# Kernel tuning notes

Hardware: AMD Instinct MI355X
Metric: run time of the kernel (lower is better)

## Reference

```python
import jax, jax.numpy as jnp
import numpy as np

B, IN, OUT, NC, S = 4096, 512, 512, 64, 1


def setup_inputs() -> dict:
    key = jax.random.key(0)
    k = jax.random.split(key, 5)
    x = jax.random.normal(k[0], (B, IN), dtype=jnp.float32)
    centers = jax.random.normal(k[1], (NC, IN), dtype=jnp.float32)
    log_sigma = jnp.zeros((NC,), dtype=jnp.float32)
    coeff_mean = jax.random.normal(k[2], (IN, OUT, NC), dtype=jnp.float32) * 0.05
    coeff_log_var = jnp.full((IN, OUT, NC), -5.0, dtype=jnp.float32)
    base_weight = jax.random.normal(k[3], (IN, OUT), dtype=jnp.float32) * 0.05
    eps = jax.random.normal(k[4], (S, IN, OUT, NC), dtype=jnp.float32)
    return {"x": x, "centers": centers, "log_sigma": log_sigma,
            "coeff_mean": coeff_mean, "coeff_log_var": coeff_log_var,
            "base_weight": base_weight, "eps": eps}


def reference(x, centers, log_sigma, coeff_mean, coeff_log_var, base_weight, eps):
    # RBF basis: (B, NC). Original repeats this along in_features, but the
    # einsum 'bin,ion->bo' with an i-constant basis equals rbf @ coeffs.sum(i).
    dist_sq = jnp.sum((x[:, None, :] - centers[None, :, :]) ** 2, axis=-1)  # (B, NC)
    sigma = jnp.exp(log_sigma)  # (NC,)
    rbf = jnp.exp(-dist_sq / (2.0 * sigma ** 2 + 1e-8))  # (B, NC)

    # Sampled variational coefficients, reparameterized.
    std = jnp.exp(0.5 * coeff_log_var)
    coeffs = coeff_mean + eps * std            # (S, IN, OUT, NC)
    c_sum = coeffs.sum(axis=1)                 # (S, OUT, NC): sum over in_features
    n_samples = eps.shape[0]
    rbf_out = jnp.einsum('bn,son->bo', rbf, c_sum) / n_samples  # mean over samples

    out = rbf_out + x @ base_weight

    # KL vs N(0, 1) prior (prior_scale = 1.0): log(var/prior_var) = coeff_log_var
    var = jnp.exp(coeff_log_var)
    kl = 0.5 * jnp.sum(var + coeff_mean ** 2 - 1.0 - coeff_log_var)
    return out, kl
```

## Files before the change

### kernel.cpp

```cpp
#include <hip/hip_runtime.h>
#include <hip/hip_bf16.h>

#define B_SZ  4096
#define IN_F  512
#define OUT_F 512
#define NC    64
#define PAIRS 32768
#define TOT   (IN_F * PAIRS)
#define KTOT  (IN_F + NC)

typedef __attribute__((ext_vector_type(8))) short bf16x8;
typedef __attribute__((ext_vector_type(4))) float f32x4;

static __device__ inline unsigned short f2bf(float f) {
    __hip_bfloat16 h = __float2bfloat16(f);
    return *(unsigned short*)&h;
}

__global__ __launch_bounds__(1024)
void k1_partial(const float* __restrict__ cm,
                const float* __restrict__ clv,
                const float* __restrict__ eps,
                float* __restrict__ csum,
                float* __restrict__ klpart,
                int S) {
    int pb = blockIdx.x & 7;
    int rc = blockIdx.x >> 3;
    int p4 = pb * 4096 + (threadIdx.x << 2);
    size_t base = (size_t)(rc * 8) * PAIRS + p4;
    float Sf = (float)S;

    f32x4 M[8], LV[8], ES[8];
#pragma unroll
    for (int ii = 0; ii < 8; ++ii)
        M[ii] = __builtin_nontemporal_load((const f32x4*)(cm + base + (size_t)ii * PAIRS));
#pragma unroll
    for (int ii = 0; ii < 8; ++ii)
        LV[ii] = __builtin_nontemporal_load((const f32x4*)(clv + base + (size_t)ii * PAIRS));
#pragma unroll
    for (int ii = 0; ii < 8; ++ii)
        ES[ii] = __builtin_nontemporal_load((const f32x4*)(eps + base + (size_t)ii * PAIRS));
    for (int si = 1; si < S; ++si)
#pragma unroll
        for (int ii = 0; ii < 8; ++ii) {
            f32x4 e = __builtin_nontemporal_load(
                (const f32x4*)(eps + (size_t)si * TOT + base + (size_t)ii * PAIRS));
            ES[ii] += e;
        }

    f32x4 s = {0.f, 0.f, 0.f, 0.f};
    float klp = 0.f;
#pragma unroll
    for (int ii = 0; ii < 8; ++ii) {
        float e1x = __expf(0.5f * LV[ii].x);
        float e1y = __expf(0.5f * LV[ii].y);
        float e1z = __expf(0.5f * LV[ii].z);
        float e1w = __expf(0.5f * LV[ii].w);
        s.x += Sf * M[ii].x + ES[ii].x * e1x;
        s.y += Sf * M[ii].y + ES[ii].y * e1y;
        s.z += Sf * M[ii].z + ES[ii].z * e1z;
        s.w += Sf * M[ii].w + ES[ii].w * e1w;
        klp += (e1x*e1x + M[ii].x*M[ii].x - 1.f - LV[ii].x);
        klp += (e1y*e1y + M[ii].y*M[ii].y - 1.f - LV[ii].y);
        klp += (e1z*e1z + M[ii].z*M[ii].z - 1.f - LV[ii].z);
        klp += (e1w*e1w + M[ii].w*M[ii].w - 1.f - LV[ii].w);
    }

    atomicAdd(&csum[p4 + 0], s.x);
    atomicAdd(&csum[p4 + 1], s.y);
    atomicAdd(&csum[p4 + 2], s.z);
    atomicAdd(&csum[p4 + 3], s.w);

    for (int off = 32; off; off >>= 1)
        klp += __shfl_down(klp, off, 64);
    __shared__ float wsum[16];
    if ((threadIdx.x & 63) == 0) wsum[threadIdx.x >> 6] = klp;
    __syncthreads();
    if (threadIdx.x == 0) {
        float t = 0.f;
#pragma unroll
        for (int i = 0; i < 16; ++i) t += wsum[i];
        klpart[blockIdx.x] = t;
    }
}

__global__ __launch_bounds__(512)
void k_mid(const float* __restrict__ x,
           const float* __restrict__ centers,
           const float* __restrict__ log_sigma,
           const float* __restrict__ csum,
           const float* __restrict__ klpart,
           const float* __restrict__ bw,
           unsigned short* __restrict__ rbf,
           unsigned short* __restrict__ wct,
           unsigned short* __restrict__ xbf,
           float* __restrict__ kl_out,
           float inv_S) {
    __shared__ float shbuf[16 * 8 * 64];
    int bid = blockIdx.x, t = threadIdx.x;

    if (bid < 256) {
        float (*red)[8][64] = (float (*)[8][64])shbuf;
        int n = t & 63;
        int wu = __builtin_amdgcn_readfirstlane(t >> 6);
        int b0 = bid * 16;

        float creg[64];
#pragma unroll
        for (int q = 0; q < 16; ++q) {
            float4 v = *(const float4*)(centers + (size_t)n * IN_F + wu * 64 + q * 4);
            creg[q * 4 + 0] = v.x; creg[q * 4 + 1] = v.y;
            creg[q * 4 + 2] = v.z; creg[q * 4 + 3] = v.w;
        }

        float dacc[16];
#pragma unroll
        for (int bi = 0; bi < 16; ++bi) {
            const float* xr = x + (size_t)(b0 + bi) * IN_F + wu * 64;
            float d0 = 0.f, d1 = 0.f, d2 = 0.f, d3 = 0.f;
#pragma unroll
            for (int j = 0; j < 64; j += 4) {
                float t0 = xr[j + 0] - creg[j + 0];
                float t1 = xr[j + 1] - creg[j + 1];
                float t2 = xr[j + 2] - creg[j + 2];
                float t3 = xr[j + 3] - creg[j + 3];
                d0 = fmaf(t0, t0, d0); d1 = fmaf(t1, t1, d1);
                d2 = fmaf(t2, t2, d2); d3 = fmaf(t3, t3, d3);
            }
            dacc[bi] = (d0 + d1) + (d2 + d3);
        }
#pragma unroll
        for (int bi = 0; bi < 16; ++bi)
            red[bi][wu][n] = dacc[bi];
        __syncthreads();
#pragma unroll
        for (int pass = 0; pass < 2; ++pass) {
            int idx = pass * 512 + t;
            int bi = idx >> 6, nn = idx & 63;
            float ssum = 0.f;
#pragma unroll
            for (int w = 0; w < 8; ++w) ssum += red[bi][w][nn];
            float sg  = __expf(log_sigma[nn]);
            float inv = 1.f / (2.f * sg * sg + 1e-8f);
            rbf[(size_t)(b0 + bi) * NC + nn] = f2bf(__expf(-ssum * inv));
        }
    } else if (bid < 320) {
        float* tile = shbuf;
        int bb = bid - 256;
        int bi = bb >> 3, bj = bb & 7;
        int cq = t & 15, rq = t >> 4;
#pragma unroll
        for (int rr = 0; rr < 2; ++rr) {
            int row = rq * 2 + rr;
            float4 v = *(const float4*)(bw + (size_t)(bi * 64 + row) * OUT_F + bj * 64 + cq * 4);
            *(float4*)&tile[row * 68 + cq * 4] = v;
        }
        __syncthreads();
#pragma unroll
        for (int rr = 0; rr < 2; ++rr) {
            int orow = rq * 2 + rr;
            ushort4 w;
            w.x = f2bf(tile[(cq * 4 + 0) * 68 + orow]);
            w.y = f2bf(tile[(cq * 4 + 1) * 68 + orow]);
            w.z = f2bf(tile[(cq * 4 + 2) * 68 + orow]);
            w.w = f2bf(tile[(cq * 4 + 3) * 68 + orow]);
            *(ushort4*)(wct + (size_t)(bj * 64 + orow) * KTOT + bi * 64 + cq * 4) = w;
        }
    } else if (bid < 384) {
        size_t base = (size_t)(bid - 320) * 32768;
#pragma unroll
        for (int q = 0; q < 16; ++q) {
            size_t off = base + q * 2048 + t * 4;
            float4 v = *(const float4*)(x + off);
            ushort4 w = {f2bf(v.x), f2bf(v.y), f2bf(v.z), f2bf(v.w)};
            *(ushort4*)(xbf + off) = w;
        }
    } else if (bid == 384) {
        float v = klpart[t];
        for (int off = 32; off; off >>= 1)
            v += __shfl_down(v, off, 64);
        float* wsum = shbuf;
        if ((t & 63) == 0) wsum[t >> 6] = v;
        __syncthreads();
        if (t == 0) {
            float s = 0.f;
#pragma unroll
            for (int i = 0; i < 8; ++i) s += wsum[i];
            kl_out[0] = 0.5f * s;
        }
    } else {
        int p4 = (bid - 385) * 2048 + t * 4;
        float4 a = *(const float4*)(csum + p4);
        int o = p4 >> 6, n = p4 & 63;
        ushort4 w;
        w.x = f2bf(a.x * inv_S);
        w.y = f2bf(a.y * inv_S);
        w.z = f2bf(a.z * inv_S);
        w.w = f2bf(a.w * inv_S);
        *(ushort4*)(wct + (size_t)o * KTOT + IN_F + n) = w;
    }
}

__global__ __launch_bounds__(256)
void k3_mfma(const unsigned short* __restrict__ xbf,
             const unsigned short* __restrict__ rbf,
             const unsigned short* __restrict__ wct,
             float* __restrict__ out) {
    __shared__ __align__(16) unsigned short As[64 * 72];
    __shared__ __align__(16) unsigned short Bs[64 * 72];
    int t = threadIdx.x;
    int bm = blockIdx.x >> 3, bn = blockIdx.x & 7;
    int b0 = bm * 64, o0 = bn * 64;
    int ar = t & 63, ah = t >> 6;
    int lane = t & 63, wv = t >> 6;
    int fm = lane & 15, kg = lane >> 4;

    f32x4 acc[4] = {{0,0,0,0},{0,0,0,0},{0,0,0,0},{0,0,0,0}};
    const int abase = (wv * 16 + fm) * 72 + kg * 8;
    const int soff  = ar * 72 + ah * 16;

    for (int it = 0; it < 9; ++it) {
        bf16x8 av0, av1, bv0, bv1;
        if (it < 8) {
            int k0 = it * 64;
            av0 = *(const bf16x8*)(xbf + (size_t)(b0 + ar) * IN_F + k0 + ah * 16);
            av1 = *(const bf16x8*)(xbf + (size_t)(b0 + ar) * IN_F + k0 + ah * 16 + 8);
            bv0 = *(const bf16x8*)(wct + (size_t)(o0 + ar) * KTOT + k0 + ah * 16);
            bv1 = *(const bf16x8*)(wct + (size_t)(o0 + ar) * KTOT + k0 + ah * 16 + 8);
        } else {
            av0 = *(const bf16x8*)(rbf + (size_t)(b0 + ar) * NC + ah * 16);
            av1 = *(const bf16x8*)(rbf + (size_t)(b0 + ar) * NC + ah * 16 + 8);
            bv0 = *(const bf16x8*)(wct + (size_t)(o0 + ar) * KTOT + IN_F + ah * 16);
            bv1 = *(const bf16x8*)(wct + (size_t)(o0 + ar) * KTOT + IN_F + ah * 16 + 8);
        }
        __syncthreads();
        *(bf16x8*)&As[soff]     = av0;
        *(bf16x8*)&As[soff + 8] = av1;
        *(bf16x8*)&Bs[soff]     = bv0;
        *(bf16x8*)&Bs[soff + 8] = bv1;
        __syncthreads();
        bf16x8 af0 = *(bf16x8*)&As[abase];
        bf16x8 af1 = *(bf16x8*)&As[abase + 32];
#pragma unroll
        for (int nf = 0; nf < 4; ++nf) {
            bf16x8 b0f = *(bf16x8*)&Bs[(nf * 16 + fm) * 72 + kg * 8];
            acc[nf] = __builtin_amdgcn_mfma_f32_16x16x32_bf16(af0, b0f, acc[nf], 0, 0, 0);
            bf16x8 b1f = *(bf16x8*)&Bs[(nf * 16 + fm) * 72 + 32 + kg * 8];
            acc[nf] = __builtin_amdgcn_mfma_f32_16x16x32_bf16(af1, b1f, acc[nf], 0, 0, 0);
        }
    }

#pragma unroll
    for (int nf = 0; nf < 4; ++nf)
#pragma unroll
        for (int rr = 0; rr < 4; ++rr)
            out[(size_t)(b0 + wv * 16 + kg * 4 + rr) * OUT_F + o0 + nf * 16 + fm] = acc[nf][rr];
}

extern "C" void kernel_launch(void* const* d_in, const int* in_sizes, int n_in,
                              void* d_out, int out_size, void* d_ws, size_t ws_size,
                              hipStream_t stream) {
    const float* x         = (const float*)d_in[0];
    const float* centers   = (const float*)d_in[1];
    const float* log_sigma = (const float*)d_in[2];
    const float* cm        = (const float*)d_in[3];
    const float* clv       = (const float*)d_in[4];
    const float* bw        = (const float*)d_in[5];
    const float* eps       = (const float*)d_in[6];

    float* out = (float*)d_out;
    float* kl  = out + (size_t)B_SZ * OUT_F;

    float* csum   = (float*)d_ws;
    float* klpart = csum + PAIRS;
    unsigned short* wct = (unsigned short*)(klpart + 512);
    unsigned short* rbf = wct + (size_t)OUT_F * KTOT;
    unsigned short* xbf = rbf + (size_t)B_SZ * NC;

    int S = in_sizes[6] / TOT;

    hipMemsetAsync(csum, 0, PAIRS * sizeof(float), stream);
    k1_partial<<<512, 1024, 0, stream>>>(cm, clv, eps, csum, klpart, S);
    k_mid<<<401, 512, 0, stream>>>(x, centers, log_sigma, csum, klpart, bw,
                                   rbf, wct, xbf, kl, 1.0f / (float)S);
    k3_mfma<<<(B_SZ / 64) * (OUT_F / 64), 256, 0, stream>>>(xbf, rbf, wct, out);
}
```

Before: 269.4 us.

## Replace atomic accumulation of coefficient sums with per-chunk partials reduced in mid kernel

The first kernel no longer atomically adds into a zeroed coefficient-sum buffer. Each block now covers 16 input rows in two groups of 8 and writes a plain partial sum for its chunk (32 chunks) to workspace. The middle kernel gains 64 blocks that reduce the 32 partials per pair and write bf16 weights, and the memset launch goes away. This removes atomic contention and one launch, but adds about 4 MB of partial writes and reads, uses more workspace, and halves the first kernel's block size.

New measurement: 235.3 us. 12.7% less time.

```diff
diff --git a/kernel.cpp b/kernel.cpp
--- a/kernel.cpp
+++ b/kernel.cpp
@@ -8,6 +8,7 @@
 #define PAIRS 32768
 #define TOT   (IN_F * PAIRS)
 #define KTOT  (IN_F + NC)
+#define RCH   32
 
 typedef __attribute__((ext_vector_type(8))) short bf16x8;
 typedef __attribute__((ext_vector_type(4))) float f32x4;
@@ -17,69 +18,69 @@
     return *(unsigned short*)&h;
 }
 
-__global__ __launch_bounds__(1024)
+__global__ __launch_bounds__(512)
 void k1_partial(const float* __restrict__ cm,
                 const float* __restrict__ clv,
                 const float* __restrict__ eps,
-                float* __restrict__ csum,
+                float* __restrict__ part,
                 float* __restrict__ klpart,
                 int S) {
-    int pb = blockIdx.x & 7;
-    int rc = blockIdx.x >> 3;
-    int p4 = pb * 4096 + (threadIdx.x << 2);
-    size_t base = (size_t)(rc * 8) * PAIRS + p4;
+    int pb = blockIdx.x & 15;
+    int rc = blockIdx.x >> 4;
+    int p4 = pb * 2048 + (threadIdx.x << 2);
     float Sf = (float)S;
-
-    f32x4 M[8], LV[8], ES[8];
-#pragma unroll
-    for (int ii = 0; ii < 8; ++ii)
-        M[ii] = __builtin_nontemporal_load((const f32x4*)(cm + base + (size_t)ii * PAIRS));
-#pragma unroll
-    for (int ii = 0; ii < 8; ++ii)
-        LV[ii] = __builtin_nontemporal_load((const f32x4*)(clv + base + (size_t)ii * PAIRS));
-#pragma unroll
-    for (int ii = 0; ii < 8; ++ii)
-        ES[ii] = __builtin_nontemporal_load((const f32x4*)(eps + base + (size_t)ii * PAIRS));
-    for (int si = 1; si < S; ++si)
-#pragma unroll
-        for (int ii = 0; ii < 8; ++ii) {
-            f32x4 e = __builtin_nontemporal_load(
-                (const f32x4*)(eps + (size_t)si * TOT + base + (size_t)ii * PAIRS));
-            ES[ii] += e;
-        }
 
     f32x4 s = {0.f, 0.f, 0.f, 0.f};
     float klp = 0.f;
-#pragma unroll
-    for (int ii = 0; ii < 8; ++ii) {
-        float e1x = __expf(0.5f * LV[ii].x);
-        float e1y = __expf(0.5f * LV[ii].y);
-        float e1z = __expf(0.5f * LV[ii].z);
-        float e1w = __expf(0.5f * LV[ii].w);
-        s.x += Sf * M[ii].x + ES[ii].x * e1x;
-        s.y += Sf * M[ii].y + ES[ii].y * e1y;
-        s.z += Sf * M[ii].z + ES[ii].z * e1z;
-        s.w += Sf * M[ii].w + ES[ii].w * e1w;
-        klp += (e1x*e1x + M[ii].x*M[ii].x - 1.f - LV[ii].x);
-        klp += (e1y*e1y + M[ii].y*M[ii].y - 1.f - LV[ii].y);
-        klp += (e1z*e1z + M[ii].z*M[ii].z - 1.f - LV[ii].z);
-        klp += (e1w*e1w + M[ii].w*M[ii].w - 1.f - LV[ii].w);
-    }
-
-    atomicAdd(&csum[p4 + 0], s.x);
-    atomicAdd(&csum[p4 + 1], s.y);
-    atomicAdd(&csum[p4 + 2], s.z);
-    atomicAdd(&csum[p4 + 3], s.w);
+
+    for (int g = 0; g < 2; ++g) {
+        size_t base = (size_t)(rc * 16 + g * 8) * PAIRS + p4;
+        f32x4 M[8], LV[8], ES[8];
+#pragma unroll
+        for (int ii = 0; ii < 8; ++ii)
+            M[ii] = __builtin_nontemporal_load((const f32x4*)(cm + base + (size_t)ii * PAIRS));
+#pragma unroll
+        for (int ii = 0; ii < 8; ++ii)
+            LV[ii] = __builtin_nontemporal_load((const f32x4*)(clv + base + (size_t)ii * PAIRS));
+#pragma unroll
+        for (int ii = 0; ii < 8; ++ii)
+            ES[ii] = __builtin_nontemporal_load((const f32x4*)(eps + base + (size_t)ii * PAIRS));
+        for (int si = 1; si < S; ++si)
+#pragma unroll
+            for (int ii = 0; ii < 8; ++ii) {
+                f32x4 e = __builtin_nontemporal_load(
+                    (const f32x4*)(eps + (size_t)si * TOT + base + (size_t)ii * PAIRS));
+                ES[ii] += e;
+            }
+
+#pragma unroll
+        for (int ii = 0; ii < 8; ++ii) {
+            float e1x = __expf(0.5f * LV[ii].x);
+            float e1y = __expf(0.5f * LV[ii].y);
+            float e1z = __expf(0.5f * LV[ii].z);
+            float e1w = __expf(0.5f * LV[ii].w);
+            s.x += Sf * M[ii].x + ES[ii].x * e1x;
+            s.y += Sf * M[ii].y + ES[ii].y * e1y;
+            s.z += Sf * M[ii].z + ES[ii].z * e1z;
+            s.w += Sf * M[ii].w + ES[ii].w * e1w;
+            klp += (e1x*e1x + M[ii].x*M[ii].x - 1.f - LV[ii].x);
+            klp += (e1y*e1y + M[ii].y*M[ii].y - 1.f - LV[ii].y);
+            klp += (e1z*e1z + M[ii].z*M[ii].z - 1.f - LV[ii].z);
+            klp += (e1w*e1w + M[ii].w*M[ii].w - 1.f - LV[ii].w);
+        }
+    }
+
+    *(f32x4*)(part + (size_t)rc * PAIRS + p4) = s;
 
     for (int off = 32; off; off >>= 1)
         klp += __shfl_down(klp, off, 64);
-    __shared__ float wsum[16];
+    __shared__ float wsum[8];
     if ((threadIdx.x & 63) == 0) wsum[threadIdx.x >> 6] = klp;
     __syncthreads();
     if (threadIdx.x == 0) {
         float t = 0.f;
 #pragma unroll
-        for (int i = 0; i < 16; ++i) t += wsum[i];
+        for (int i = 0; i < 8; ++i) t += wsum[i];
         klpart[blockIdx.x] = t;
     }
 }
@@ -88,7 +89,7 @@
 void k_mid(const float* __restrict__ x,
            const float* __restrict__ centers,
            const float* __restrict__ log_sigma,
-           const float* __restrict__ csum,
+           const float* __restrict__ part,
            const float* __restrict__ klpart,
            const float* __restrict__ bw,
            unsigned short* __restrict__ rbf,
@@ -145,8 +146,20 @@
             rbf[(size_t)(b0 + bi) * NC + nn] = f2bf(__expf(-ssum * inv));
         }
     } else if (bid < 320) {
+        int p = (bid - 256) * 512 + t;
+        float a0 = 0.f, a1 = 0.f, a2 = 0.f, a3 = 0.f;
+#pragma unroll
+        for (int r = 0; r < RCH; r += 4) {
+            a0 += part[(size_t)(r + 0) * PAIRS + p];
+            a1 += part[(size_t)(r + 1) * PAIRS + p];
+            a2 += part[(size_t)(r + 2) * PAIRS + p];
+            a3 += part[(size_t)(r + 3) * PAIRS + p];
+        }
+        int o = p >> 6, n = p & 63;
+        wct[(size_t)o * KTOT + IN_F + n] = f2bf(((a0 + a1) + (a2 + a3)) * inv_S);
+    } else if (bid < 384) {
         float* tile = shbuf;
-        int bb = bid - 256;
+        int bb = bid - 320;
         int bi = bb >> 3, bj = bb & 7;
         int cq = t & 15, rq = t >> 4;
 #pragma unroll
@@ -166,15 +179,6 @@
             w.w = f2bf(tile[(cq * 4 + 3) * 68 + orow]);
             *(ushort4*)(wct + (size_t)(bj * 64 + orow) * KTOT + bi * 64 + cq * 4) = w;
         }
-    } else if (bid < 384) {
-        size_t base = (size_t)(bid - 320) * 32768;
-#pragma unroll
-        for (int q = 0; q < 16; ++q) {
-            size_t off = base + q * 2048 + t * 4;
-            float4 v = *(const float4*)(x + off);
-            ushort4 w = {f2bf(v.x), f2bf(v.y), f2bf(v.z), f2bf(v.w)};
-            *(ushort4*)(xbf + off) = w;
-        }
     } else if (bid == 384) {
         float v = klpart[t];
         for (int off = 32; off; off >>= 1)
@@ -189,15 +193,14 @@
             kl_out[0] = 0.5f * s;
         }
     } else {
-        int p4 = (bid - 385) * 2048 + t * 4;
-        float4 a = *(const float4*)(csum + p4);
-        int o = p4 >> 6, n = p4 & 63;
-        ushort4 w;
-        w.x = f2bf(a.x * inv_S);
-        w.y = f2bf(a.y * inv_S);
-        w.z = f2bf(a.z * inv_S);
-        w.w = f2bf(a.w * inv_S);
-        *(ushort4*)(wct + (size_t)o * KTOT + IN_F + n) = w;
+        size_t base = (size_t)(bid - 385) * 32768;
+#pragma unroll
+        for (int q = 0; q < 16; ++q) {
+            size_t off = base + q * 2048 + t * 4;
+            float4 v = *(const float4*)(x + off);
+            ushort4 w = {f2bf(v.x), f2bf(v.y), f2bf(v.z), f2bf(v.w)};
+            *(ushort4*)(xbf + off) = w;
+        }
     }
 }
 
@@ -271,17 +274,16 @@
     float* out = (float*)d_out;
     float* kl  = out + (size_t)B_SZ * OUT_F;
 
-    float* csum   = (float*)d_ws;
-    float* klpart = csum + PAIRS;
+    float* part   = (float*)d_ws;
+    float* klpart = part + (size_t)RCH * PAIRS;
     unsigned short* wct = (unsigned short*)(klpart + 512);
     unsigned short* rbf = wct + (size_t)OUT_F * KTOT;
     unsigned short* xbf = rbf + (size_t)B_SZ * NC;
 
     int S = in_sizes[6] / TOT;
 
-    hipMemsetAsync(csum, 0, PAIRS * sizeof(float), stream);
-    k1_partial<<<512, 1024, 0, stream>>>(cm, clv, eps, csum, klpart, S);
-    k_mid<<<401, 512, 0, stream>>>(x, centers, log_sigma, csum, klpart, bw,
+    k1_partial<<<512, 512, 0, stream>>>(cm, clv, eps, part, klpart, S);
+    k_mid<<<449, 512, 0, stream>>>(x, centers, log_sigma, part, klpart, bw,
                                    rbf, wct, xbf, kl, 1.0f / (float)S);
     k3_mfma<<<(B_SZ / 64) * (OUT_F / 64), 256, 0, stream>>>(xbf, rbf, wct, out);
 }
```
